# Optimization experiments

Hardware: AMD Instinct MI355X
Metric: run time of the kernel (lower is better)

## Reference

```python
import jax, jax.numpy as jnp
import numpy as np

B, LS, LL = 1024, 128, 2048
E, VOCAB = 16, 160000
NH, KD = 8, 6
LSH_DIM, TOPK = 16, 48
D_ITEM = 3 * E  # 48
EPS = 1e-3  # keras LayerNormalization default epsilon


def setup_inputs() -> dict:
    key = jax.random.key(0)
    ks = iter(jax.random.split(key, 64))
    def nk():
        return next(ks)
    def ids(shape):
        return jax.random.randint(nk(), shape, 0, VOCAB, dtype=jnp.int32)
    inp = {}
    for n in ['uid', 'utag1', 'utag2', 'utag3', 'utag4',
              'label_goods_ids', 'label_shop_ids', 'label_cate_ids']:
        inp[n] = ids((B,))
    for n in ['shortterm_goods_ids', 'shortterm_shop_ids', 'shortterm_cate_ids']:
        inp[n] = ids((B, LS))
    for n in ['longterm_goods_ids', 'longterm_shop_ids', 'longterm_cate_ids']:
        inp[n] = ids((B, LL))
    def rn(shape, s=0.05):
        return (jax.random.normal(nk(), shape) * s).astype(jnp.float32)
    inp['emb_table'] = rn((VOCAB, E))
    inp['H'] = rn((D_ITEM, LSH_DIM), 1.0)  # non-trainable random projection
    for p in ('s', 'l'):
        inp[p + 'Wq'] = rn((D_ITEM, NH, KD)); inp[p + 'bq'] = jnp.zeros((NH, KD), jnp.float32)
        inp[p + 'Wk'] = rn((D_ITEM, NH, KD)); inp[p + 'bk'] = jnp.zeros((NH, KD), jnp.float32)
        inp[p + 'Wv'] = rn((D_ITEM, NH, KD)); inp[p + 'bv'] = jnp.zeros((NH, KD), jnp.float32)
        inp[p + 'Wo'] = rn((NH, KD, D_ITEM)); inp[p + 'bo'] = jnp.zeros((D_ITEM,), jnp.float32)
    Din = D_ITEM + 5 * E + D_ITEM + D_ITEM  # 224
    inp['W1'] = rn((Din, 200)); inp['b1'] = jnp.zeros((200,), jnp.float32)
    inp['g1'] = jnp.ones((200,), jnp.float32); inp['be1'] = jnp.zeros((200,), jnp.float32)
    inp['W2'] = rn((200, 80)); inp['b2'] = jnp.zeros((80,), jnp.float32)
    inp['g2'] = jnp.ones((80,), jnp.float32); inp['be2'] = jnp.zeros((80,), jnp.float32)
    inp['W3'] = rn((80, 1)); inp['b3'] = jnp.zeros((1,), jnp.float32)
    return inp


def _ln(x, g, b):
    m = jnp.mean(x, axis=-1, keepdims=True)
    v = jnp.mean((x - m) ** 2, axis=-1, keepdims=True)
    return (x - m) * jax.lax.rsqrt(v + EPS) * g + b


def _mha(q, kv, mask3, Wq, bq, Wk, bk, Wv, bv, Wo, bo):
    # q: [B,1,D], kv: [B,K,D], mask3: [B,1,K] float (1=keep)
    qh = jnp.einsum('bqe,ehd->bqhd', q, Wq) + bq
    kh = jnp.einsum('bke,ehd->bkhd', kv, Wk) + bk
    vh = jnp.einsum('bke,ehd->bkhd', kv, Wv) + bv
    sc = jnp.einsum('bqhd,bkhd->bhqk', qh, kh) / jnp.sqrt(jnp.float32(KD))
    sc = sc + (1.0 - mask3[:, None, :, :]) * jnp.float32(-1e9)
    a = jax.nn.softmax(sc, axis=-1)
    o = jnp.einsum('bhqk,bkhd->bqhd', a, vh)
    return jnp.einsum('bqhd,hde->bqe', o, Wo) + bo


def reference(uid, utag1, utag2, utag3, utag4,
              label_goods_ids, label_shop_ids, label_cate_ids,
              shortterm_goods_ids, shortterm_shop_ids, shortterm_cate_ids,
              longterm_goods_ids, longterm_shop_ids, longterm_cate_ids,
              emb_table, H,
              sWq, sbq, sWk, sbk, sWv, sbv, sWo, sbo,
              lWq, lbq, lWk, lbk, lWv, lbv, lWo, lbo,
              W1, b1, g1, be1, W2, b2, g2, be2, W3, b3):
    short_mask = shortterm_goods_ids == 0  # padding_index == 0
    long_mask = longterm_goods_ids == 0

    def stack_embed(lst):
        X = jnp.stack([t if t.ndim == 2 else t[:, None] for t in lst], axis=2)  # [B,L,F]
        Xe = emb_table[X]  # [B,L,F,E]
        return Xe.reshape(Xe.shape[0], Xe.shape[1], -1)

    X_item = stack_embed([label_goods_ids, label_shop_ids, label_cate_ids])  # [B,1,48]
    X_user = stack_embed([uid, utag1, utag2, utag3, utag4])                  # [B,1,80]
    X_short = stack_embed([shortterm_goods_ids, shortterm_shop_ids, shortterm_cate_ids])  # [B,LS,48]
    X_long = stack_embed([longterm_goods_ids, longterm_shop_ids, longterm_cate_ids])      # [B,LL,48]

    # short-term interest
    slen = jnp.sum((~short_mask).astype(jnp.int32), axis=1)
    smask = (jnp.arange(LS)[None, :] < slen[:, None]).astype(jnp.float32)[:, None, :]
    short_int = _mha(X_item, X_short, smask, sWq, sbq, sWk, sbk, sWv, sbv, sWo, sbo)[:, 0]

    # long-term interest: LSH sign-hash hamming top-k retrieval
    series_codes = jnp.sign(jnp.einsum('ble,em->blm', X_long, H))  # [B,LL,16]
    item_codes = jnp.sign(jnp.einsum('ble,em->blm', X_item, H))    # [B,1,16]
    scores = jnp.sum((series_codes == item_codes).astype(jnp.float32), axis=-1)  # [B,LL]
    scores = jnp.where(long_mask, -jnp.inf, scores)
    _, idx = jax.lax.top_k(scores, TOPK)  # descending, padded entries last
    top_emb = jnp.take_along_axis(X_long, idx[:, :, None], axis=1)  # [B,TOPK,48]
    top_mask = jnp.take_along_axis(long_mask, idx, axis=1)
    llen = jnp.sum((~top_mask).astype(jnp.int32), axis=1)
    lmask = (jnp.arange(TOPK)[None, :] < llen[:, None]).astype(jnp.float32)[:, None, :]
    long_int = _mha(X_item, top_emb, lmask, lWq, lbq, lWk, lbk, lWv, lbv, lWo, lbo)[:, 0]

    x = jnp.concatenate([X_item[:, 0], X_user[:, 0], short_int, long_int], axis=1)  # [B,224]
    h1 = jax.nn.relu(_ln(x @ W1 + b1, g1, be1))
    h2 = jax.nn.relu(_ln(h1 @ W2 + b2, g2, be2))
    out = jax.nn.sigmoid(h2 @ W3 + b3)  # [B,1]
    return out
```

## Files before the change

### kernel.cpp

```cpp
#include <hip/hip_runtime.h>
#include <math.h>

#define BB 1024
#define LSx 128
#define LLx 2048
#define TOPKx 48

__global__ __launch_bounds__(256, 2) void k_score(
    const int* __restrict__ lg, const int* __restrict__ lsh, const int* __restrict__ lc,
    const int* __restrict__ ig, const int* __restrict__ ish, const int* __restrict__ ici,
    const float* __restrict__ emb, const float* __restrict__ Hm,
    signed char* __restrict__ gsc)
{
  __shared__ float Xitem[48];
  __shared__ int icode[16];
  __shared__ __align__(16) float4 xsh[256][5];
  const int b = blockIdx.y, tid = threadIdx.x;

  const int l = blockIdx.x * 256 + tid;
  const size_t off = (size_t)b * LLx + l;
  const int gid = lg[off];

  if (tid < 48) {
    const int seg = tid >> 4, e = tid & 15;
    const int id = (seg == 0) ? ig[b] : (seg == 1) ? ish[b] : ici[b];
    Xitem[tid] = emb[(size_t)id * 16 + e];
  }
  __syncthreads();
  if (tid < 16) {
    float dd = 0.f;
    for (int e = 0; e < 48; ++e) dd += Xitem[e] * Hm[e * 16 + tid];
    icode[tid] = (dd > 0.f) ? 1 : (dd < 0.f ? -1 : 0);
  }

  const int srow = tid >> 2;
  const int q = tid & 3;
  const size_t bbase = (size_t)b * LLx + (size_t)blockIdx.x * 256;

  float d[16];
  #pragma unroll
  for (int m = 0; m < 16; ++m) d[m] = 0.f;

  #pragma unroll
  for (int seg = 0; seg < 3; ++seg) {
    const int* idarr = (seg == 0) ? lg : (seg == 1) ? lsh : lc;
    #pragma unroll
    for (int jj = 0; jj < 4; ++jj) {
      const int pos = jj * 64 + srow;
      const int id = idarr[bbase + pos];
      xsh[pos][q] = *(const float4*)(emb + (size_t)id * 16 + q * 4);
    }
    __syncthreads();
    if (gid != 0) {
      float x[16];
      #pragma unroll
      for (int qq = 0; qq < 4; ++qq) {
        const float4 r = xsh[tid][qq];
        x[qq * 4 + 0] = r.x; x[qq * 4 + 1] = r.y;
        x[qq * 4 + 2] = r.z; x[qq * 4 + 3] = r.w;
      }
      const float* hb = Hm + seg * 256;
      #pragma unroll
      for (int i = 0; i < 16; ++i) {
        const float xi = x[i];
        #pragma unroll
        for (int mc = 0; mc < 4; ++mc) {
          const float4 h4 = *(const float4*)(hb + i * 16 + mc * 4);
          d[mc * 4 + 0] += xi * h4.x;
          d[mc * 4 + 1] += xi * h4.y;
          d[mc * 4 + 2] += xi * h4.z;
          d[mc * 4 + 3] += xi * h4.w;
        }
      }
    }
    if (seg < 2) __syncthreads();
  }

  int sc = -1;
  if (gid != 0) {
    sc = 0;
    #pragma unroll
    for (int m = 0; m < 16; ++m) {
      const int cs = (d[m] > 0.f) ? 1 : (d[m] < 0.f ? -1 : 0);
      sc += (cs == icode[m]) ? 1 : 0;
    }
  }
  gsc[off] = (signed char)sc;
}

__global__ __launch_bounds__(256) void k_topk(
    const signed char* __restrict__ gsc, int* __restrict__ sel)
{
  __shared__ int hist[18];
  __shared__ int cnt_above;
  __shared__ int wsum[4];
  const int b = blockIdx.x, tid = threadIdx.x;

  const int2 myv = ((const int2*)(gsc + (size_t)b * LLx))[tid];
  signed char loc[8];
  *(int2*)loc = myv;

  if (tid < 18) hist[tid] = 0;
  if (tid == 0) cnt_above = 0;
  __syncthreads();

  #pragma unroll
  for (int j = 0; j < 8; ++j) atomicAdd(&hist[(int)loc[j] + 1], 1);
  __syncthreads();

  int above = 0, tval = -1, need = 0;
  for (int s = 16; s >= -1; --s) {
    const int c = hist[s + 1];
    if (above + c >= TOPKx) { tval = s; need = TOPKx - above; break; }
    above += c;
  }

  const int base_l = tid * (LLx / 256);
  int cnt = 0;
  #pragma unroll
  for (int j = 0; j < 8; ++j) cnt += ((int)loc[j] == tval) ? 1 : 0;
  int v = cnt;
  const int lane = tid & 63, wave = tid >> 6;
  #pragma unroll
  for (int o = 1; o < 64; o <<= 1) {
    const int u = __shfl_up(v, o, 64);
    if (lane >= o) v += u;
  }
  if (lane == 63) wsum[wave] = v;
  __syncthreads();
  int rank = v - cnt;
  for (int w = 0; w < wave; ++w) rank += wsum[w];

  #pragma unroll
  for (int j = 0; j < 8; ++j) {
    const int l = base_l + j;
    const int s = (int)loc[j];
    if (s > tval) {
      const int slot = atomicAdd(&cnt_above, 1);
      sel[b * TOPKx + slot] = l;
    } else if (s == tval) {
      if (rank < need) sel[b * TOPKx + above + rank] = l;
      ++rank;
    }
  }
}

template<int K, int STRIDE, bool IS_LONG>
__global__ __launch_bounds__(128) void k_mha(
    const int* __restrict__ kg, const int* __restrict__ ks, const int* __restrict__ kc,
    const int* __restrict__ ig, const int* __restrict__ ish, const int* __restrict__ ici,
    const float* __restrict__ emb,
    const float* __restrict__ Wq, const float* __restrict__ bq,
    const float* __restrict__ Wk, const float* __restrict__ bk,
    const float* __restrict__ Wv, const float* __restrict__ bv,
    const float* __restrict__ Wo, const float* __restrict__ bo,
    const int* __restrict__ sel,
    float* __restrict__ outv)
{
  __shared__ float Xitem[48];
  __shared__ float qh[48];
  __shared__ __align__(16) float vhs[K][48];
  __shared__ float scs[8][K + 4];
  __shared__ float osm[48];
  __shared__ unsigned char validf[K];
  const int b = blockIdx.x, tid = threadIdx.x;

  if (tid < 48) {
    const int seg = tid >> 4, e = tid & 15;
    const int id = (seg == 0) ? ig[b] : (seg == 1) ? ish[b] : ici[b];
    Xitem[tid] = emb[(size_t)id * 16 + e];
  }
  __syncthreads();
  if (tid < 48) {
    float a = bq[tid];
    for (int e = 0; e < 48; ++e) a += Xitem[e] * Wq[e * 48 + tid];
    qh[tid] = a;
  }

  int gid = 0, sid = 0, cid = 0;
  if (tid < K) {
    const int pos = IS_LONG ? sel[b * TOPKx + tid] : tid;
    const size_t off = (size_t)b * STRIDE + pos;
    gid = kg[off]; sid = ks[off]; cid = kc[off];
  }
  const int nval = __syncthreads_count((tid < K) && (gid != 0));

  if (tid < K) {
    validf[tid] = IS_LONG ? (unsigned char)(gid != 0) : (unsigned char)(tid < nval);
    float kh[48], vh[48];
    #pragma unroll
    for (int j = 0; j < 48; ++j) { kh[j] = bk[j]; vh[j] = bv[j]; }
    const int ids3[3] = {gid, sid, cid};
    #pragma unroll
    for (int seg = 0; seg < 3; ++seg) {
      const float* row = emb + (size_t)ids3[seg] * 16;
      #pragma unroll
      for (int i4 = 0; i4 < 4; ++i4) {
        const float4 xv = ((const float4*)row)[i4];
        const float xs[4] = {xv.x, xv.y, xv.z, xv.w};
        #pragma unroll
        for (int c = 0; c < 4; ++c) {
          const int e = seg * 16 + i4 * 4 + c;
          const float* wkr = Wk + e * 48;
          const float* wvr = Wv + e * 48;
          const float xe = xs[c];
          #pragma unroll
          for (int j = 0; j < 48; ++j) {
            kh[j] += xe * wkr[j];
            vh[j] += xe * wvr[j];
          }
        }
      }
    }
    #pragma unroll
    for (int h = 0; h < 8; ++h) {
      float s = 0.f;
      #pragma unroll
      for (int d = 0; d < 6; ++d) s += qh[h * 6 + d] * kh[h * 6 + d];
      scs[h][tid] = s * 0.40824829046386301637f;
    }
    #pragma unroll
    for (int j = 0; j < 48; ++j) vhs[tid][j] = vh[j];
  }
  __syncthreads();

  {
    const int h = tid >> 4, l16 = tid & 15;
    float amax = -INFINITY;
    for (int k = l16; k < K; k += 16) if (validf[k]) amax = fmaxf(amax, scs[h][k]);
    #pragma unroll
    for (int m = 1; m < 16; m <<= 1) amax = fmaxf(amax, __shfl_xor(amax, m, 16));
    if (nval == 0) {
      for (int k = l16; k < K; k += 16) scs[h][k] = 1.0f / (float)K;
    } else {
      float ssum = 0.f;
      for (int k = l16; k < K; k += 16) {
        const float ev = validf[k] ? expf(scs[h][k] - amax) : 0.f;
        scs[h][k] = ev;
        ssum += ev;
      }
      #pragma unroll
      for (int m = 1; m < 16; m <<= 1) ssum += __shfl_xor(ssum, m, 16);
      const float inv = 1.0f / ssum;
      for (int k = l16; k < K; k += 16) scs[h][k] *= inv;
    }
  }
  __syncthreads();

  if (tid < 48) {
    const int h = tid / 6;
    float a = 0.f;
    for (int k = 0; k < K; ++k) a += scs[h][k] * vhs[k][tid];
    osm[tid] = a;
  }
  __syncthreads();
  if (tid < 48) {
    float r = bo[tid];
    for (int j = 0; j < 48; ++j) r += osm[j] * Wo[j * 48 + tid];
    outv[b * 48 + tid] = r;
  }
}

__device__ __forceinline__ float block_sum256(float v, float* red) {
  #pragma unroll
  for (int m = 32; m >= 1; m >>= 1) v += __shfl_xor(v, m, 64);
  const int lane = threadIdx.x & 63, wave = threadIdx.x >> 6;
  if (lane == 0) red[wave] = v;
  __syncthreads();
  const float t = red[0] + red[1] + red[2] + red[3];
  __syncthreads();
  return t;
}

__global__ __launch_bounds__(256) void k_mlp(
    const int* __restrict__ uid, const int* __restrict__ u1, const int* __restrict__ u2,
    const int* __restrict__ u3, const int* __restrict__ u4,
    const int* __restrict__ ig, const int* __restrict__ ish, const int* __restrict__ ici,
    const float* __restrict__ emb,
    const float* __restrict__ sint, const float* __restrict__ lint,
    const float* __restrict__ W1, const float* __restrict__ b1,
    const float* __restrict__ g1, const float* __restrict__ be1,
    const float* __restrict__ W2, const float* __restrict__ b2,
    const float* __restrict__ g2, const float* __restrict__ be2,
    const float* __restrict__ W3, const float* __restrict__ b3,
    float* __restrict__ out)
{
  __shared__ __align__(16) float x[224];
  __shared__ __align__(16) float h1[200];
  __shared__ float h2[80];
  __shared__ float red[4];
  const int b = blockIdx.x, tid = threadIdx.x;

  if (tid < 128) {
    const int e = tid & 15;
    int id;
    if (tid < 48) {
      const int seg = tid >> 4;
      id = (seg == 0) ? ig[b] : (seg == 1) ? ish[b] : ici[b];
    } else {
      const int f = (tid - 48) >> 4;
      id = (f == 0) ? uid[b] : (f == 1) ? u1[b] : (f == 2) ? u2[b] : (f == 3) ? u3[b] : u4[b];
    }
    x[tid] = emb[(size_t)id * 16 + e];
  } else if (tid < 176) {
    x[tid] = sint[b * 48 + (tid - 128)];
  } else if (tid < 224) {
    x[tid] = lint[b * 48 + (tid - 176)];
  }
  __syncthreads();

  float v = 0.f;
  if (tid < 200) {
    v = b1[tid];
    for (int i4 = 0; i4 < 56; ++i4) {
      const float4 xv = *(const float4*)(x + i4 * 4);
      const float* w = W1 + i4 * 4 * 200 + tid;
      v += xv.x * w[0];
      v += xv.y * w[200];
      v += xv.z * w[400];
      v += xv.w * w[600];
    }
  }
  const float mean1 = block_sum256((tid < 200) ? v : 0.f, red) * (1.0f / 200.0f);
  const float dv = (tid < 200) ? (v - mean1) : 0.f;
  const float var1 = block_sum256(dv * dv, red) * (1.0f / 200.0f);
  if (tid < 200) {
    const float y = (v - mean1) * rsqrtf(var1 + 1e-3f) * g1[tid] + be1[tid];
    h1[tid] = fmaxf(y, 0.f);
  }
  __syncthreads();

  float v2 = 0.f;
  if (tid < 80) {
    v2 = b2[tid];
    for (int i4 = 0; i4 < 50; ++i4) {
      const float4 xv = *(const float4*)(h1 + i4 * 4);
      const float* w = W2 + i4 * 4 * 80 + tid;
      v2 += xv.x * w[0];
      v2 += xv.y * w[80];
      v2 += xv.z * w[160];
      v2 += xv.w * w[240];
    }
  }
  const float mean2 = block_sum256((tid < 80) ? v2 : 0.f, red) * (1.0f / 80.0f);
  const float dv2 = (tid < 80) ? (v2 - mean2) : 0.f;
  const float var2 = block_sum256(dv2 * dv2, red) * (1.0f / 80.0f);
  if (tid < 80) {
    const float y = (v2 - mean2) * rsqrtf(var2 + 1e-3f) * g2[tid] + be2[tid];
    h2[tid] = fmaxf(y, 0.f);
  }
  __syncthreads();

  const float p = (tid < 80) ? h2[tid] * W3[tid] : 0.f;
  const float z = block_sum256(p, red);
  if (tid == 0) {
    out[b] = 1.0f / (1.0f + expf(-(z + b3[0])));
  }
}

extern "C" void kernel_launch(void* const* d_in, const int* in_sizes, int n_in,
                              void* d_out, int out_size, void* d_ws, size_t ws_size,
                              hipStream_t stream) {
  (void)in_sizes; (void)n_in; (void)out_size; (void)ws_size;
  const int* uid = (const int*)d_in[0];
  const int* u1  = (const int*)d_in[1];
  const int* u2  = (const int*)d_in[2];
  const int* u3  = (const int*)d_in[3];
  const int* u4  = (const int*)d_in[4];
  const int* ig  = (const int*)d_in[5];
  const int* ish = (const int*)d_in[6];
  const int* ici = (const int*)d_in[7];
  const int* sg  = (const int*)d_in[8];
  const int* ss  = (const int*)d_in[9];
  const int* scd = (const int*)d_in[10];
  const int* lg  = (const int*)d_in[11];
  const int* ls  = (const int*)d_in[12];
  const int* lcd = (const int*)d_in[13];
  const float* emb = (const float*)d_in[14];
  const float* Hm  = (const float*)d_in[15];
  const float* sWq = (const float*)d_in[16];
  const float* sbq = (const float*)d_in[17];
  const float* sWk = (const float*)d_in[18];
  const float* sbk = (const float*)d_in[19];
  const float* sWv = (const float*)d_in[20];
  const float* sbv = (const float*)d_in[21];
  const float* sWo = (const float*)d_in[22];
  const float* sbo = (const float*)d_in[23];
  const float* lWq = (const float*)d_in[24];
  const float* lbq = (const float*)d_in[25];
  const float* lWk = (const float*)d_in[26];
  const float* lbk = (const float*)d_in[27];
  const float* lWv = (const float*)d_in[28];
  const float* lbv = (const float*)d_in[29];
  const float* lWo = (const float*)d_in[30];
  const float* lbo = (const float*)d_in[31];
  const float* W1 = (const float*)d_in[32];
  const float* b1 = (const float*)d_in[33];
  const float* g1 = (const float*)d_in[34];
  const float* be1 = (const float*)d_in[35];
  const float* W2 = (const float*)d_in[36];
  const float* b2 = (const float*)d_in[37];
  const float* g2 = (const float*)d_in[38];
  const float* be2 = (const float*)d_in[39];
  const float* W3 = (const float*)d_in[40];
  const float* b3 = (const float*)d_in[41];
  float* out = (float*)d_out;

  signed char* gsc = (signed char*)d_ws;
  int* sel = (int*)((char*)d_ws + (size_t)BB * LLx);
  float* sint = (float*)(sel + BB * TOPKx);
  float* lint = sint + BB * 48;

  k_score<<<dim3(LLx / 256, BB), dim3(256), 0, stream>>>(
      lg, ls, lcd, ig, ish, ici, emb, Hm, gsc);
  k_topk<<<dim3(BB), dim3(256), 0, stream>>>(gsc, sel);
  k_mha<128, 128, false><<<dim3(BB), dim3(128), 0, stream>>>(
      sg, ss, scd, ig, ish, ici, emb,
      sWq, sbq, sWk, sbk, sWv, sbv, sWo, sbo, (const int*)nullptr, sint);
  k_mha<48, 2048, true><<<dim3(BB), dim3(128), 0, stream>>>(
      lg, ls, lcd, ig, ish, ici, emb,
      lWq, lbq, lWk, lbk, lWv, lbv, lWo, lbo, sel, lint);
  k_mlp<<<dim3(BB), dim3(256), 0, stream>>>(
      uid, u1, u2, u3, u4, ig, ish, ici, emb,
      sint, lint, W1, b1, g1, be1, W2, b2, g2, be2, W3, b3, out);
}
```

Baseline: 327.9 us.

## Fuse top-k, both attention blocks and MLP into one per-batch kernel

Merges k_topk, the short and long k_mha launches and k_mlp into a single 256-thread kernel per batch row. Threads 0-127 handle short-term attention while threads 128-175 handle long-term attention in parallel. Selected indices and the attention outputs now stay in shared memory instead of round-tripping through global workspace. This removes three launches and the intermediate global traffic, but raises shared-memory and register use per block, which may lower occupancy, and leaves the long-attention half of the block mostly idle.

```diff
diff --git a/kernel.cpp b/kernel.cpp
--- a/kernel.cpp
+++ b/kernel.cpp
@@ -88,24 +88,93 @@
   gsc[off] = (signed char)sc;
 }
 
-__global__ __launch_bounds__(256) void k_topk(
-    const signed char* __restrict__ gsc, int* __restrict__ sel)
+__device__ __forceinline__ float block_sum256(float v, float* red) {
+  #pragma unroll
+  for (int m = 32; m >= 1; m >>= 1) v += __shfl_xor(v, m, 64);
+  const int lane = threadIdx.x & 63, wave = threadIdx.x >> 6;
+  if (lane == 0) red[wave] = v;
+  __syncthreads();
+  const float t = red[0] + red[1] + red[2] + red[3];
+  __syncthreads();
+  return t;
+}
+
+__global__ __launch_bounds__(256) void k_fused(
+    const int* __restrict__ sg, const int* __restrict__ ss, const int* __restrict__ scd,
+    const int* __restrict__ lg, const int* __restrict__ ls, const int* __restrict__ lcd,
+    const int* __restrict__ ig, const int* __restrict__ ish, const int* __restrict__ ici,
+    const int* __restrict__ uid, const int* __restrict__ u1, const int* __restrict__ u2,
+    const int* __restrict__ u3, const int* __restrict__ u4,
+    const float* __restrict__ emb,
+    const float* __restrict__ sWq, const float* __restrict__ sbq,
+    const float* __restrict__ sWk, const float* __restrict__ sbk,
+    const float* __restrict__ sWv, const float* __restrict__ sbv,
+    const float* __restrict__ sWo, const float* __restrict__ sbo,
+    const float* __restrict__ lWq, const float* __restrict__ lbq,
+    const float* __restrict__ lWk, const float* __restrict__ lbk,
+    const float* __restrict__ lWv, const float* __restrict__ lbv,
+    const float* __restrict__ lWo, const float* __restrict__ lbo,
+    const signed char* __restrict__ gsc,
+    const float* __restrict__ W1, const float* __restrict__ b1,
+    const float* __restrict__ g1, const float* __restrict__ be1,
+    const float* __restrict__ W2, const float* __restrict__ b2,
+    const float* __restrict__ g2, const float* __restrict__ be2,
+    const float* __restrict__ W3, const float* __restrict__ b3,
+    float* __restrict__ out)
 {
-  __shared__ int hist[18];
+  __shared__ float Xitem[48];
+  __shared__ float qh_s[48], qh_l[48];
+  __shared__ __align__(16) float vhs_s[LSx][48];
+  __shared__ float scs_s[8][LSx + 4];
+  __shared__ __align__(16) float vhs_l[TOPKx][48];
+  __shared__ float scs_l[8][TOPKx + 4];
+  __shared__ float osm_s[48], osm_l[48];
+  __shared__ unsigned char validf_s[LSx];
+  __shared__ unsigned char validf_l[TOPKx];
+  __shared__ int hist[18], wsum[4], nv[4], selsh[TOPKx];
   __shared__ int cnt_above;
-  __shared__ int wsum[4];
+  __shared__ __align__(16) float x[224];
+  __shared__ __align__(16) float h1[200];
+  __shared__ float h2[80];
+  __shared__ float red[4];
+
   const int b = blockIdx.x, tid = threadIdx.x;
+  const bool shorth = tid < 128;
+  const int t = shorth ? tid : tid - 128;
 
   const int2 myv = ((const int2*)(gsc + (size_t)b * LLx))[tid];
   signed char loc[8];
   *(int2*)loc = myv;
 
+  if (tid < 48) {
+    const int seg = tid >> 4, e = tid & 15;
+    const int id = (seg == 0) ? ig[b] : (seg == 1) ? ish[b] : ici[b];
+    Xitem[tid] = emb[(size_t)id * 16 + e];
+  }
+  if (tid >= 160 && tid < 240) {
+    const int u = tid - 160;
+    const int f = u >> 4;
+    const int id = (f == 0) ? uid[b] : (f == 1) ? u1[b] : (f == 2) ? u2[b]
+                 : (f == 3) ? u3[b] : u4[b];
+    x[48 + u] = emb[(size_t)id * 16 + (u & 15)];
+  }
   if (tid < 18) hist[tid] = 0;
   if (tid == 0) cnt_above = 0;
   __syncthreads();
 
   #pragma unroll
   for (int j = 0; j < 8; ++j) atomicAdd(&hist[(int)loc[j] + 1], 1);
+  if (tid < 48) {
+    float a = sbq[tid];
+    for (int e = 0; e < 48; ++e) a += Xitem[e] * sWq[e * 48 + tid];
+    qh_s[tid] = a;
+  } else if (tid >= 64 && tid < 112) {
+    x[tid - 64] = Xitem[tid - 64];
+  } else if (tid >= 128 && tid < 176) {
+    float a = lbq[t];
+    for (int e = 0; e < 48; ++e) a += Xitem[e] * lWq[e * 48 + t];
+    qh_l[t] = a;
+  }
   __syncthreads();
 
   int above = 0, tval = -1, need = 0;
@@ -114,7 +183,6 @@
     if (above + c >= TOPKx) { tval = s; need = TOPKx - above; break; }
     above += c;
   }
-
   const int base_l = tid * (LLx / 256);
   int cnt = 0;
   #pragma unroll
@@ -137,59 +205,33 @@
     const int s = (int)loc[j];
     if (s > tval) {
       const int slot = atomicAdd(&cnt_above, 1);
-      sel[b * TOPKx + slot] = l;
+      selsh[slot] = l;
     } else if (s == tval) {
-      if (rank < need) sel[b * TOPKx + above + rank] = l;
+      if (rank < need) selsh[above + rank] = l;
       ++rank;
     }
   }
-}
-
-template<int K, int STRIDE, bool IS_LONG>
-__global__ __launch_bounds__(128) void k_mha(
-    const int* __restrict__ kg, const int* __restrict__ ks, const int* __restrict__ kc,
-    const int* __restrict__ ig, const int* __restrict__ ish, const int* __restrict__ ici,
-    const float* __restrict__ emb,
-    const float* __restrict__ Wq, const float* __restrict__ bq,
-    const float* __restrict__ Wk, const float* __restrict__ bk,
-    const float* __restrict__ Wv, const float* __restrict__ bv,
-    const float* __restrict__ Wo, const float* __restrict__ bo,
-    const int* __restrict__ sel,
-    float* __restrict__ outv)
-{
-  __shared__ float Xitem[48];
-  __shared__ float qh[48];
-  __shared__ __align__(16) float vhs[K][48];
-  __shared__ float scs[8][K + 4];
-  __shared__ float osm[48];
-  __shared__ unsigned char validf[K];
-  const int b = blockIdx.x, tid = threadIdx.x;
-
-  if (tid < 48) {
-    const int seg = tid >> 4, e = tid & 15;
-    const int id = (seg == 0) ? ig[b] : (seg == 1) ? ish[b] : ici[b];
-    Xitem[tid] = emb[(size_t)id * 16 + e];
-  }
-  __syncthreads();
-  if (tid < 48) {
-    float a = bq[tid];
-    for (int e = 0; e < 48; ++e) a += Xitem[e] * Wq[e * 48 + tid];
-    qh[tid] = a;
-  }
+  __syncthreads();
 
   int gid = 0, sid = 0, cid = 0;
-  if (tid < K) {
-    const int pos = IS_LONG ? sel[b * TOPKx + tid] : tid;
-    const size_t off = (size_t)b * STRIDE + pos;
-    gid = kg[off]; sid = ks[off]; cid = kc[off];
-  }
-  const int nval = __syncthreads_count((tid < K) && (gid != 0));
-
-  if (tid < K) {
-    validf[tid] = IS_LONG ? (unsigned char)(gid != 0) : (unsigned char)(tid < nval);
+  if (shorth) {
+    const size_t off = (size_t)b * LSx + t;
+    gid = sg[off]; sid = ss[off]; cid = scd[off];
+  } else if (t < TOPKx) {
+    const int pos = selsh[t];
+    const size_t off = (size_t)b * LLx + pos;
+    gid = lg[off]; sid = ls[off]; cid = lcd[off];
+  }
+  const unsigned long long bal = __ballot(gid != 0);
+  if ((tid & 63) == 0) nv[tid >> 6] = __popcll(bal);
+  __syncthreads();
+  const int nval = shorth ? (nv[0] + nv[1]) : (nv[2] + nv[3]);
+
+  if (shorth) {
+    validf_s[t] = (unsigned char)(t < nval);
     float kh[48], vh[48];
     #pragma unroll
-    for (int j = 0; j < 48; ++j) { kh[j] = bk[j]; vh[j] = bv[j]; }
+    for (int j = 0; j < 48; ++j) { kh[j] = sbk[j]; vh[j] = sbv[j]; }
     const int ids3[3] = {gid, sid, cid};
     #pragma unroll
     for (int seg = 0; seg < 3; ++seg) {
@@ -201,8 +243,8 @@
         #pragma unroll
         for (int c = 0; c < 4; ++c) {
           const int e = seg * 16 + i4 * 4 + c;
-          const float* wkr = Wk + e * 48;
-          const float* wvr = Wv + e * 48;
+          const float* wkr = sWk + e * 48;
+          const float* wvr = sWv + e * 48;
           const float xe = xs[c];
           #pragma unroll
           for (int j = 0; j < 48; ++j) {
@@ -216,33 +258,90 @@
     for (int h = 0; h < 8; ++h) {
       float s = 0.f;
       #pragma unroll
-      for (int d = 0; d < 6; ++d) s += qh[h * 6 + d] * kh[h * 6 + d];
-      scs[h][tid] = s * 0.40824829046386301637f;
-    }
-    #pragma unroll
-    for (int j = 0; j < 48; ++j) vhs[tid][j] = vh[j];
+      for (int d = 0; d < 6; ++d) s += qh_s[h * 6 + d] * kh[h * 6 + d];
+      scs_s[h][t] = s * 0.40824829046386301637f;
+    }
+    #pragma unroll
+    for (int j = 0; j < 48; ++j) vhs_s[t][j] = vh[j];
+  } else if (t < TOPKx) {
+    validf_l[t] = (unsigned char)(gid != 0);
+    float kh[48], vh[48];
+    #pragma unroll
+    for (int j = 0; j < 48; ++j) { kh[j] = lbk[j]; vh[j] = lbv[j]; }
+    const int ids3[3] = {gid, sid, cid};
+    #pragma unroll
+    for (int seg = 0; seg < 3; ++seg) {
+      const float* row = emb + (size_t)ids3[seg] * 16;
+      #pragma unroll
+      for (int i4 = 0; i4 < 4; ++i4) {
+        const float4 xv = ((const float4*)row)[i4];
+        const float xs[4] = {xv.x, xv.y, xv.z, xv.w};
+        #pragma unroll
+        for (int c = 0; c < 4; ++c) {
+          const int e = seg * 16 + i4 * 4 + c;
+          const float* wkr = lWk + e * 48;
+          const float* wvr = lWv + e * 48;
+          const float xe = xs[c];
+          #pragma unroll
+          for (int j = 0; j < 48; ++j) {
+            kh[j] += xe * wkr[j];
+            vh[j] += xe * wvr[j];
+          }
+        }
+      }
+    }
+    #pragma unroll
+    for (int h = 0; h < 8; ++h) {
+      float s = 0.f;
+      #pragma unroll
+      for (int d = 0; d < 6; ++d) s += qh_l[h * 6 + d] * kh[h * 6 + d];
+      scs_l[h][t] = s * 0.40824829046386301637f;
+    }
+    #pragma unroll
+    for (int j = 0; j < 48; ++j) vhs_l[t][j] = vh[j];
   }
   __syncthreads();
 
   {
-    const int h = tid >> 4, l16 = tid & 15;
-    float amax = -INFINITY;
-    for (int k = l16; k < K; k += 16) if (validf[k]) amax = fmaxf(amax, scs[h][k]);
-    #pragma unroll
-    for (int m = 1; m < 16; m <<= 1) amax = fmaxf(amax, __shfl_xor(amax, m, 16));
-    if (nval == 0) {
-      for (int k = l16; k < K; k += 16) scs[h][k] = 1.0f / (float)K;
+    const int h = t >> 4, l16 = t & 15;
+    if (shorth) {
+      float amax = -INFINITY;
+      for (int k = l16; k < LSx; k += 16) if (validf_s[k]) amax = fmaxf(amax, scs_s[h][k]);
+      #pragma unroll
+      for (int m = 1; m < 16; m <<= 1) amax = fmaxf(amax, __shfl_xor(amax, m, 16));
+      if (nval == 0) {
+        for (int k = l16; k < LSx; k += 16) scs_s[h][k] = 1.0f / (float)LSx;
+      } else {
+        float ssum = 0.f;
+        for (int k = l16; k < LSx; k += 16) {
+          const float ev = validf_s[k] ? expf(scs_s[h][k] - amax) : 0.f;
+          scs_s[h][k] = ev;
+          ssum += ev;
+        }
+        #pragma unroll
+        for (int m = 1; m < 16; m <<= 1) ssum += __shfl_xor(ssum, m, 16);
+        const float inv = 1.0f / ssum;
+        for (int k = l16; k < LSx; k += 16) scs_s[h][k] *= inv;
+      }
     } else {
-      float ssum = 0.f;
-      for (int k = l16; k < K; k += 16) {
-        const float ev = validf[k] ? expf(scs[h][k] - amax) : 0.f;
-        scs[h][k] = ev;
-        ssum += ev;
-      }
-      #pragma unroll
-      for (int m = 1; m < 16; m <<= 1) ssum += __shfl_xor(ssum, m, 16);
-      const float inv = 1.0f / ssum;
-      for (int k = l16; k < K; k += 16) scs[h][k] *= inv;
+      float amax = -INFINITY;
+      for (int k = l16; k < TOPKx; k += 16) if (validf_l[k]) amax = fmaxf(amax, scs_l[h][k]);
+      #pragma unroll
+      for (int m = 1; m < 16; m <<= 1) amax = fmaxf(amax, __shfl_xor(amax, m, 16));
+      if (nval == 0) {
+        for (int k = l16; k < TOPKx; k += 16) scs_l[h][k] = 1.0f / (float)TOPKx;
+      } else {
+        float ssum = 0.f;
+        for (int k = l16; k < TOPKx; k += 16) {
+          const float ev = validf_l[k] ? expf(scs_l[h][k] - amax) : 0.f;
+          scs_l[h][k] = ev;
+          ssum += ev;
+        }
+        #pragma unroll
+        for (int m = 1; m < 16; m <<= 1) ssum += __shfl_xor(ssum, m, 16);
+        const float inv = 1.0f / ssum;
+        for (int k = l16; k < TOPKx; k += 16) scs_l[h][k] *= inv;
+      }
     }
   }
   __syncthreads();
@@ -250,82 +349,44 @@
   if (tid < 48) {
     const int h = tid / 6;
     float a = 0.f;
-    for (int k = 0; k < K; ++k) a += scs[h][k] * vhs[k][tid];
-    osm[tid] = a;
-  }
-  __syncthreads();
+    for (int k = 0; k < LSx; ++k) a += scs_s[h][k] * vhs_s[k][tid];
+    osm_s[tid] = a;
+  } else if (!shorth && t < 48) {
+    const int h = t / 6;
+    float a = 0.f;
+    for (int k = 0; k < TOPKx; ++k) a += scs_l[h][k] * vhs_l[k][t];
+    osm_l[t] = a;
+  }
+  __syncthreads();
+
   if (tid < 48) {
-    float r = bo[tid];
-    for (int j = 0; j < 48; ++j) r += osm[j] * Wo[j * 48 + tid];
-    outv[b * 48 + tid] = r;
-  }
-}
-
-__device__ __forceinline__ float block_sum256(float v, float* red) {
-  #pragma unroll
-  for (int m = 32; m >= 1; m >>= 1) v += __shfl_xor(v, m, 64);
-  const int lane = threadIdx.x & 63, wave = threadIdx.x >> 6;
-  if (lane == 0) red[wave] = v;
-  __syncthreads();
-  const float t = red[0] + red[1] + red[2] + red[3];
-  __syncthreads();
-  return t;
-}
-
-__global__ __launch_bounds__(256) void k_mlp(
-    const int* __restrict__ uid, const int* __restrict__ u1, const int* __restrict__ u2,
-    const int* __restrict__ u3, const int* __restrict__ u4,
-    const int* __restrict__ ig, const int* __restrict__ ish, const int* __restrict__ ici,
-    const float* __restrict__ emb,
-    const float* __restrict__ sint, const float* __restrict__ lint,
-    const float* __restrict__ W1, const float* __restrict__ b1,
-    const float* __restrict__ g1, const float* __restrict__ be1,
-    const float* __restrict__ W2, const float* __restrict__ b2,
-    const float* __restrict__ g2, const float* __restrict__ be2,
-    const float* __restrict__ W3, const float* __restrict__ b3,
-    float* __restrict__ out)
-{
-  __shared__ __align__(16) float x[224];
-  __shared__ __align__(16) float h1[200];
-  __shared__ float h2[80];
-  __shared__ float red[4];
-  const int b = blockIdx.x, tid = threadIdx.x;
-
-  if (tid < 128) {
-    const int e = tid & 15;
-    int id;
-    if (tid < 48) {
-      const int seg = tid >> 4;
-      id = (seg == 0) ? ig[b] : (seg == 1) ? ish[b] : ici[b];
-    } else {
-      const int f = (tid - 48) >> 4;
-      id = (f == 0) ? uid[b] : (f == 1) ? u1[b] : (f == 2) ? u2[b] : (f == 3) ? u3[b] : u4[b];
-    }
-    x[tid] = emb[(size_t)id * 16 + e];
-  } else if (tid < 176) {
-    x[tid] = sint[b * 48 + (tid - 128)];
-  } else if (tid < 224) {
-    x[tid] = lint[b * 48 + (tid - 176)];
-  }
-  __syncthreads();
-
-  float v = 0.f;
+    float r = sbo[tid];
+    for (int j = 0; j < 48; ++j) r += osm_s[j] * sWo[j * 48 + tid];
+    x[128 + tid] = r;
+  } else if (!shorth && t < 48) {
+    float r = lbo[t];
+    for (int j = 0; j < 48; ++j) r += osm_l[j] * lWo[j * 48 + t];
+    x[176 + t] = r;
+  }
+  __syncthreads();
+
+  float v1 = 0.f;
   if (tid < 200) {
-    v = b1[tid];
+    v1 = b1[tid];
     for (int i4 = 0; i4 < 56; ++i4) {
       const float4 xv = *(const float4*)(x + i4 * 4);
       const float* w = W1 + i4 * 4 * 200 + tid;
-      v += xv.x * w[0];
-      v += xv.y * w[200];
-      v += xv.z * w[400];
-      v += xv.w * w[600];
-    }
-  }
-  const float mean1 = block_sum256((tid < 200) ? v : 0.f, red) * (1.0f / 200.0f);
-  const float dv = (tid < 200) ? (v - mean1) : 0.f;
+      v1 += xv.x * w[0];
+      v1 += xv.y * w[200];
+      v1 += xv.z * w[400];
+      v1 += xv.w * w[600];
+    }
+  }
+  const float mean1 = block_sum256((tid < 200) ? v1 : 0.f, red) * (1.0f / 200.0f);
+  const float dv = (tid < 200) ? (v1 - mean1) : 0.f;
   const float var1 = block_sum256(dv * dv, red) * (1.0f / 200.0f);
   if (tid < 200) {
-    const float y = (v - mean1) * rsqrtf(var1 + 1e-3f) * g1[tid] + be1[tid];
+    const float y = (v1 - mean1) * rsqrtf(var1 + 1e-3f) * g1[tid] + be1[tid];
     h1[tid] = fmaxf(y, 0.f);
   }
   __syncthreads();
@@ -407,20 +468,14 @@
   float* out = (float*)d_out;
 
   signed char* gsc = (signed char*)d_ws;
-  int* sel = (int*)((char*)d_ws + (size_t)BB * LLx);
-  float* sint = (float*)(sel + BB * TOPKx);
-  float* lint = sint + BB * 48;
 
   k_score<<<dim3(LLx / 256, BB), dim3(256), 0, stream>>>(
       lg, ls, lcd, ig, ish, ici, emb, Hm, gsc);
-  k_topk<<<dim3(BB), dim3(256), 0, stream>>>(gsc, sel);
-  k_mha<128, 128, false><<<dim3(BB), dim3(128), 0, stream>>>(
-      sg, ss, scd, ig, ish, ici, emb,
-      sWq, sbq, sWk, sbk, sWv, sbv, sWo, sbo, (const int*)nullptr, sint);
-  k_mha<48, 2048, true><<<dim3(BB), dim3(128), 0, stream>>>(
-      lg, ls, lcd, ig, ish, ici, emb,
-      lWq, lbq, lWk, lbk, lWv, lbv, lWo, lbo, sel, lint);
-  k_mlp<<<dim3(BB), dim3(256), 0, stream>>>(
-      uid, u1, u2, u3, u4, ig, ish, ici, emb,
-      sint, lint, W1, b1, g1, be1, W2, b2, g2, be2, W3, b3, out);
+  k_fused<<<dim3(BB), dim3(256), 0, stream>>>(
+      sg, ss, scd, lg, ls, lcd, ig, ish, ici,
+      uid, u1, u2, u3, u4, emb,
+      sWq, sbq, sWk, sbk, sWv, sbv, sWo, sbo,
+      lWq, lbq, lWk, lbk, lWv, lbv, lWo, lbo,
+      gsc,
+      W1, b1, g1, be1, W2, b2, g2, be2, W3, b3, out);
 }
```

Measured after the change: 332.2 us. No clear change (+1.3%).

## Split MHA per head across blocks, merge short/long launches, move Wo into MLP

Applied to the files above, without the earlier changes.

The attention kernel now launches one block per (batch, head, short/long) pair in a single grid, so each thread computes only 6 K/V outputs instead of 48. That cuts register pressure and spreads the work over 16x more blocks. The output projection Wo moves into the MLP kernel, and the score kernel is reshaped to 128-thread blocks. In exchange, embedding gathers and the query projection are repeated for every head, which adds redundant memory traffic.

```diff
diff --git a/kernel.cpp b/kernel.cpp
--- a/kernel.cpp
+++ b/kernel.cpp
@@ -6,7 +6,7 @@
 #define LLx 2048
 #define TOPKx 48
 
-__global__ __launch_bounds__(256, 2) void k_score(
+__global__ __launch_bounds__(128, 4) void k_score(
     const int* __restrict__ lg, const int* __restrict__ lsh, const int* __restrict__ lc,
     const int* __restrict__ ig, const int* __restrict__ ish, const int* __restrict__ ici,
     const float* __restrict__ emb, const float* __restrict__ Hm,
@@ -14,10 +14,10 @@
 {
   __shared__ float Xitem[48];
   __shared__ int icode[16];
-  __shared__ __align__(16) float4 xsh[256][5];
+  __shared__ __align__(16) float4 xsh[128][5];
   const int b = blockIdx.y, tid = threadIdx.x;
 
-  const int l = blockIdx.x * 256 + tid;
+  const int l = blockIdx.x * 128 + tid;
   const size_t off = (size_t)b * LLx + l;
   const int gid = lg[off];
 
@@ -35,7 +35,7 @@
 
   const int srow = tid >> 2;
   const int q = tid & 3;
-  const size_t bbase = (size_t)b * LLx + (size_t)blockIdx.x * 256;
+  const size_t bbase = (size_t)b * LLx + (size_t)blockIdx.x * 128;
 
   float d[16];
   #pragma unroll
@@ -46,7 +46,7 @@
     const int* idarr = (seg == 0) ? lg : (seg == 1) ? lsh : lc;
     #pragma unroll
     for (int jj = 0; jj < 4; ++jj) {
-      const int pos = jj * 64 + srow;
+      const int pos = jj * 32 + srow;
       const int id = idarr[bbase + pos];
       xsh[pos][q] = *(const float4*)(emb + (size_t)id * 16 + q * 4);
     }
@@ -145,25 +145,36 @@
   }
 }
 
-template<int K, int STRIDE, bool IS_LONG>
 __global__ __launch_bounds__(128) void k_mha(
-    const int* __restrict__ kg, const int* __restrict__ ks, const int* __restrict__ kc,
+    const int* __restrict__ sg, const int* __restrict__ ss, const int* __restrict__ scd,
+    const int* __restrict__ lg, const int* __restrict__ ls, const int* __restrict__ lcd,
     const int* __restrict__ ig, const int* __restrict__ ish, const int* __restrict__ ici,
     const float* __restrict__ emb,
-    const float* __restrict__ Wq, const float* __restrict__ bq,
-    const float* __restrict__ Wk, const float* __restrict__ bk,
-    const float* __restrict__ Wv, const float* __restrict__ bv,
-    const float* __restrict__ Wo, const float* __restrict__ bo,
+    const float* __restrict__ sWq, const float* __restrict__ sbq,
+    const float* __restrict__ sWk, const float* __restrict__ sbk,
+    const float* __restrict__ sWv, const float* __restrict__ sbv,
+    const float* __restrict__ lWq, const float* __restrict__ lbq,
+    const float* __restrict__ lWk, const float* __restrict__ lbk,
+    const float* __restrict__ lWv, const float* __restrict__ lbv,
     const int* __restrict__ sel,
-    float* __restrict__ outv)
+    float* __restrict__ osm_s, float* __restrict__ osm_l)
 {
   __shared__ float Xitem[48];
-  __shared__ float qh[48];
-  __shared__ __align__(16) float vhs[K][48];
-  __shared__ float scs[8][K + 4];
-  __shared__ float osm[48];
-  __shared__ unsigned char validf[K];
+  __shared__ float qh[6];
+  __shared__ float scs[LSx];
+  __shared__ float vhT[6][LSx + 4];
+  __shared__ unsigned char validf[LSx];
   const int b = blockIdx.x, tid = threadIdx.x;
+  const bool is_long = blockIdx.y >= 8;
+  const int h = is_long ? (blockIdx.y - 8) : blockIdx.y;
+
+  const float* Wq = is_long ? lWq : sWq;
+  const float* bq = is_long ? lbq : sbq;
+  const float* Wk = is_long ? lWk : sWk;
+  const float* bk = is_long ? lbk : sbk;
+  const float* Wv = is_long ? lWv : sWv;
+  const float* bv = is_long ? lbv : sbv;
+  const int K = is_long ? TOPKx : LSx;
 
   if (tid < 48) {
     const int seg = tid >> 4, e = tid & 15;
@@ -171,25 +182,29 @@
     Xitem[tid] = emb[(size_t)id * 16 + e];
   }
   __syncthreads();
-  if (tid < 48) {
-    float a = bq[tid];
-    for (int e = 0; e < 48; ++e) a += Xitem[e] * Wq[e * 48 + tid];
+  if (tid < 6) {
+    const int col = h * 6 + tid;
+    float a = bq[col];
+    for (int e = 0; e < 48; ++e) a += Xitem[e] * Wq[e * 48 + col];
     qh[tid] = a;
   }
 
   int gid = 0, sid = 0, cid = 0;
+  if (!is_long) {
+    const size_t off = (size_t)b * LSx + tid;
+    gid = sg[off]; sid = ss[off]; cid = scd[off];
+  } else if (tid < TOPKx) {
+    const int pos = sel[b * TOPKx + tid];
+    const size_t off = (size_t)b * LLx + pos;
+    gid = lg[off]; sid = ls[off]; cid = lcd[off];
+  }
+  const int nval = __syncthreads_count((tid < K) && (gid != 0));
+
   if (tid < K) {
-    const int pos = IS_LONG ? sel[b * TOPKx + tid] : tid;
-    const size_t off = (size_t)b * STRIDE + pos;
-    gid = kg[off]; sid = ks[off]; cid = kc[off];
-  }
-  const int nval = __syncthreads_count((tid < K) && (gid != 0));
-
-  if (tid < K) {
-    validf[tid] = IS_LONG ? (unsigned char)(gid != 0) : (unsigned char)(tid < nval);
-    float kh[48], vh[48];
-    #pragma unroll
-    for (int j = 0; j < 48; ++j) { kh[j] = bk[j]; vh[j] = bv[j]; }
+    validf[tid] = is_long ? (unsigned char)(gid != 0) : (unsigned char)(tid < nval);
+    float kh[6], vh[6];
+    #pragma unroll
+    for (int j = 0; j < 6; ++j) { kh[j] = bk[h * 6 + j]; vh[j] = bv[h * 6 + j]; }
     const int ids3[3] = {gid, sid, cid};
     #pragma unroll
     for (int seg = 0; seg < 3; ++seg) {
@@ -201,63 +216,54 @@
         #pragma unroll
         for (int c = 0; c < 4; ++c) {
           const int e = seg * 16 + i4 * 4 + c;
-          const float* wkr = Wk + e * 48;
-          const float* wvr = Wv + e * 48;
+          const float* wkr = Wk + e * 48 + h * 6;
+          const float* wvr = Wv + e * 48 + h * 6;
           const float xe = xs[c];
           #pragma unroll
-          for (int j = 0; j < 48; ++j) {
+          for (int j = 0; j < 6; ++j) {
             kh[j] += xe * wkr[j];
             vh[j] += xe * wvr[j];
           }
         }
       }
     }
-    #pragma unroll
-    for (int h = 0; h < 8; ++h) {
-      float s = 0.f;
-      #pragma unroll
-      for (int d = 0; d < 6; ++d) s += qh[h * 6 + d] * kh[h * 6 + d];
-      scs[h][tid] = s * 0.40824829046386301637f;
-    }
-    #pragma unroll
-    for (int j = 0; j < 48; ++j) vhs[tid][j] = vh[j];
-  }
-  __syncthreads();
-
-  {
-    const int h = tid >> 4, l16 = tid & 15;
+    float s = 0.f;
+    #pragma unroll
+    for (int d = 0; d < 6; ++d) s += qh[d] * kh[d];
+    scs[tid] = s * 0.40824829046386301637f;
+    #pragma unroll
+    for (int j = 0; j < 6; ++j) vhT[j][tid] = vh[j];
+  }
+  __syncthreads();
+
+  if (tid < 16) {
+    const int l16 = tid;
     float amax = -INFINITY;
-    for (int k = l16; k < K; k += 16) if (validf[k]) amax = fmaxf(amax, scs[h][k]);
+    for (int k = l16; k < K; k += 16) if (validf[k]) amax = fmaxf(amax, scs[k]);
     #pragma unroll
     for (int m = 1; m < 16; m <<= 1) amax = fmaxf(amax, __shfl_xor(amax, m, 16));
     if (nval == 0) {
-      for (int k = l16; k < K; k += 16) scs[h][k] = 1.0f / (float)K;
+      for (int k = l16; k < K; k += 16) scs[k] = 1.0f / (float)K;
     } else {
       float ssum = 0.f;
       for (int k = l16; k < K; k += 16) {
-        const float ev = validf[k] ? expf(scs[h][k] - amax) : 0.f;
-        scs[h][k] = ev;
+        const float ev = validf[k] ? expf(scs[k] - amax) : 0.f;
+        scs[k] = ev;
         ssum += ev;
       }
       #pragma unroll
       for (int m = 1; m < 16; m <<= 1) ssum += __shfl_xor(ssum, m, 16);
       const float inv = 1.0f / ssum;
-      for (int k = l16; k < K; k += 16) scs[h][k] *= inv;
-    }
-  }
-  __syncthreads();
-
-  if (tid < 48) {
-    const int h = tid / 6;
+      for (int k = l16; k < K; k += 16) scs[k] *= inv;
+    }
+  }
+  __syncthreads();
+
+  if (tid < 6) {
     float a = 0.f;
-    for (int k = 0; k < K; ++k) a += scs[h][k] * vhs[k][tid];
-    osm[tid] = a;
-  }
-  __syncthreads();
-  if (tid < 48) {
-    float r = bo[tid];
-    for (int j = 0; j < 48; ++j) r += osm[j] * Wo[j * 48 + tid];
-    outv[b * 48 + tid] = r;
+    for (int k = 0; k < K; ++k) a += scs[k] * vhT[tid][k];
+    float* dst = is_long ? osm_l : osm_s;
+    dst[b * 48 + h * 6 + tid] = a;
   }
 }
 
@@ -277,7 +283,9 @@
     const int* __restrict__ u3, const int* __restrict__ u4,
     const int* __restrict__ ig, const int* __restrict__ ish, const int* __restrict__ ici,
     const float* __restrict__ emb,
-    const float* __restrict__ sint, const float* __restrict__ lint,
+    const float* __restrict__ osm_s, const float* __restrict__ osm_l,
+    const float* __restrict__ sWo, const float* __restrict__ sbo,
+    const float* __restrict__ lWo, const float* __restrict__ lbo,
     const float* __restrict__ W1, const float* __restrict__ b1,
     const float* __restrict__ g1, const float* __restrict__ be1,
     const float* __restrict__ W2, const float* __restrict__ b2,
@@ -289,6 +297,7 @@
   __shared__ __align__(16) float h1[200];
   __shared__ float h2[80];
   __shared__ float red[4];
+  __shared__ float osm_sl[48], osm_ll[48];
   const int b = blockIdx.x, tid = threadIdx.x;
 
   if (tid < 128) {
@@ -303,9 +312,21 @@
     }
     x[tid] = emb[(size_t)id * 16 + e];
   } else if (tid < 176) {
-    x[tid] = sint[b * 48 + (tid - 128)];
+    osm_sl[tid - 128] = osm_s[b * 48 + (tid - 128)];
   } else if (tid < 224) {
-    x[tid] = lint[b * 48 + (tid - 176)];
+    osm_ll[tid - 176] = osm_l[b * 48 + (tid - 176)];
+  }
+  __syncthreads();
+
+  if (tid < 48) {
+    float r = sbo[tid];
+    for (int j = 0; j < 48; ++j) r += osm_sl[j] * sWo[j * 48 + tid];
+    x[128 + tid] = r;
+  } else if (tid >= 64 && tid < 112) {
+    const int c = tid - 64;
+    float r = lbo[c];
+    for (int j = 0; j < 48; ++j) r += osm_ll[j] * lWo[j * 48 + c];
+    x[176 + c] = r;
   }
   __syncthreads();
 
@@ -408,19 +429,18 @@
 
   signed char* gsc = (signed char*)d_ws;
   int* sel = (int*)((char*)d_ws + (size_t)BB * LLx);
-  float* sint = (float*)(sel + BB * TOPKx);
-  float* lint = sint + BB * 48;
-
-  k_score<<<dim3(LLx / 256, BB), dim3(256), 0, stream>>>(
+  float* osm_s = (float*)(sel + BB * TOPKx);
+  float* osm_l = osm_s + BB * 48;
+
+  k_score<<<dim3(LLx / 128, BB), dim3(128), 0, stream>>>(
       lg, ls, lcd, ig, ish, ici, emb, Hm, gsc);
   k_topk<<<dim3(BB), dim3(256), 0, stream>>>(gsc, sel);
-  k_mha<128, 128, false><<<dim3(BB), dim3(128), 0, stream>>>(
-      sg, ss, scd, ig, ish, ici, emb,
-      sWq, sbq, sWk, sbk, sWv, sbv, sWo, sbo, (const int*)nullptr, sint);
-  k_mha<48, 2048, true><<<dim3(BB), dim3(128), 0, stream>>>(
-      lg, ls, lcd, ig, ish, ici, emb,
-      lWq, lbq, lWk, lbk, lWv, lbv, lWo, lbo, sel, lint);
+  k_mha<<<dim3(BB, 16), dim3(128), 0, stream>>>(
+      sg, ss, scd, lg, ls, lcd, ig, ish, ici, emb,
+      sWq, sbq, sWk, sbk, sWv, sbv,
+      lWq, lbq, lWk, lbk, lWv, lbv, sel, osm_s, osm_l);
   k_mlp<<<dim3(BB), dim3(256), 0, stream>>>(
       uid, u1, u2, u3, u4, ig, ish, ici, emb,
-      sint, lint, W1, b1, g1, be1, W2, b2, g2, be2, W3, b3, out);
-}
+      osm_s, osm_l, sWo, sbo, lWo, lbo,
+      W1, b1, g1, be1, W2, b2, g2, be2, W3, b3, out);
+}
```

Result: faster. 304.7 us (-7.1%).
